# Kernel tuning notes

Measured on AMD Instinct MI355X. Metric: run time of the kernel, lower is better.

The kernel has to match this reference:

```python
import jax, jax.numpy as jnp
import numpy as np

B, N, H = 512, 128, 256      # graphs, nodes per graph, hidden
NH, HD = 8, 32               # heads, head dim
DEG = 8
E = B * N * DEG              # 524288 edges
BN_EPS = 1e-5


def setup_inputs() -> dict:
    key = jax.random.key(0)
    ks = jax.random.split(key, 16)

    def w(k, shape):
        return jax.random.normal(k, shape, dtype=jnp.float32) * 0.02

    # intra-graph random edges: base offset per graph, local src/dst in [0, N)
    base = jnp.repeat(jnp.arange(B, dtype=jnp.int32) * N, N * DEG)
    edge_src = base + jax.random.randint(ks[1], (E,), 0, N, dtype=jnp.int32)
    edge_dst = base + jax.random.randint(ks[2], (E,), 0, N, dtype=jnp.int32)

    return {
        "h": jax.random.normal(ks[0], (B * N, H), dtype=jnp.float32),
        "edge_src": edge_src,
        "edge_dst": edge_dst,
        "gin_w1": w(ks[3], (H, H)), "gin_b1": jnp.zeros((H,), jnp.float32),
        "gin_w2": w(ks[4], (H, H)), "gin_b2": jnp.zeros((H,), jnp.float32),
        "attn_in_w": w(ks[5], (3 * H, H)), "attn_in_b": jnp.zeros((3 * H,), jnp.float32),
        "attn_out_w": w(ks[6], (H, H)), "attn_out_b": jnp.zeros((H,), jnp.float32),
        "bn_local_g": jnp.ones((H,), jnp.float32), "bn_local_b": jnp.zeros((H,), jnp.float32),
        "bn_attn_g": jnp.ones((H,), jnp.float32), "bn_attn_b": jnp.zeros((H,), jnp.float32),
        "bn_out_g": jnp.ones((H,), jnp.float32), "bn_out_b": jnp.zeros((H,), jnp.float32),
        "ffn1_w": w(ks[7], (2 * H, H)), "ffn1_b": jnp.zeros((2 * H,), jnp.float32),
        "ffn2_w": w(ks[8], (H, 2 * H)), "ffn2_b": jnp.zeros((H,), jnp.float32),
    }


def _bn(x, g, b):
    # nn.BatchNorm1d training-mode forward: batch stats over node dim, biased var
    mean = jnp.mean(x, axis=0)
    var = jnp.mean(jnp.square(x - mean), axis=0)
    return g * (x - mean) * jax.lax.rsqrt(var + BN_EPS) + b


def _mha(x, in_w, in_b, out_w, out_b):
    # x: [B, N, H]; uniform graphs -> key_padding_mask is all-valid
    qkv = x @ in_w.T + in_b                           # [B, N, 3H]
    q, k, v = jnp.split(qkv, 3, axis=-1)
    def heads(t):
        return t.reshape(B, N, NH, HD).transpose(0, 2, 1, 3)  # [B, NH, N, HD]
    q, k, v = heads(q), heads(k), heads(v)
    scores = jnp.einsum('bhqd,bhkd->bhqk', q, k) / jnp.sqrt(jnp.float32(HD))
    att = jax.nn.softmax(scores, axis=-1)
    o = jnp.einsum('bhqk,bhkd->bhqd', att, v).transpose(0, 2, 1, 3).reshape(B, N, H)
    return o @ out_w.T + out_b


def reference(h, edge_src, edge_dst,
              gin_w1, gin_b1, gin_w2, gin_b2,
              attn_in_w, attn_in_b, attn_out_w, attn_out_b,
              bn_local_g, bn_local_b, bn_attn_g, bn_attn_b, bn_out_g, bn_out_b,
              ffn1_w, ffn1_b, ffn2_w, ffn2_b):
    # --- local GIN branch: (1+eps)*h + sum_{j in N(i)} h_j, eps=0, then 2-layer MLP
    agg = jax.ops.segment_sum(h[edge_src], edge_dst, num_segments=B * N)
    z = h + agg
    h_local = jax.nn.relu(z @ gin_w1.T + gin_b1) @ gin_w2.T + gin_b2
    h_local = _bn(h + h_local, bn_local_g, bn_local_b)

    # --- global attention branch (to_dense_batch is an exact reshape here)
    h_dense = h.reshape(B, N, H)
    h_attn = _mha(h_dense, attn_in_w, attn_in_b, attn_out_w, attn_out_b).reshape(B * N, H)
    h_attn = _bn(h + h_attn, bn_attn_g, bn_attn_b)

    # --- combine + FFN + out norm
    x = h_local + h_attn
    x = x + jax.nn.relu(x @ ffn1_w.T + ffn1_b) @ ffn2_w.T + ffn2_b
    return _bn(x, bn_out_g, bn_out_b)
```

## Files before the change

kernel.cpp:

```cpp
#include <hip/hip_runtime.h>
#include <hip/hip_bf16.h>

#define B_   512
#define N_   128
#define H_   256
#define NH_  8
#define HD_  32
#define DEG_ 8
#define R_   (B_ * N_)
#define E_   (B_ * N_ * DEG_)
#define EPG_ (N_ * DEG_)

typedef unsigned short u16;
typedef unsigned int u32;

typedef __attribute__((ext_vector_type(8))) short s16x8;
typedef __attribute__((ext_vector_type(4))) float f32x4;

__device__ __forceinline__ float b2f(u16 u) {
  union { u32 i; float f; } v;
  v.i = ((u32)u) << 16;
  return v.f;
}
__device__ __forceinline__ u16 f2b(float f) {
  union { float f; u32 u; } v;
  v.f = f;
  u32 r = (v.u + 0x7fffu + ((v.u >> 16) & 1u)) >> 16;
  return (u16)r;
}
__device__ __forceinline__ void ld4b(const u16* p, float* o) {
  ushort4 v = *(const ushort4*)p;
  o[0] = b2f(v.x); o[1] = b2f(v.y); o[2] = b2f(v.z); o[3] = b2f(v.w);
}

__device__ __forceinline__ int tix(int row, int col) {
  return ((row >> 7) << 15) + (((col >> 6) & 3) << 13) + ((row & 127) << 6) +
         (((((col >> 3) & 7) ^ (row & 7))) << 3) + (col & 7);
}

__device__ __forceinline__ void glds16(const u16* g, u16* l) {
  __builtin_amdgcn_global_load_lds(
      (const __attribute__((address_space(1))) void*)g,
      (__attribute__((address_space(3))) void*)l, 16, 0, 0);
}


#define OFF_GW1 0
#define OFF_GB1 65536
#define OFF_GW2 65792
#define OFF_GB2 131328
#define OFF_AIW 131584
#define OFF_AIB 328192
#define OFF_AOW 328960
#define OFF_AOB 394496
#define OFF_F1W 394752
#define OFF_F1B 525824
#define OFF_F2W 526336
#define OFF_F2B 657408
#define W_TOTAL 657664

__global__ void zero_stats(float* __restrict__ st) {
  st[blockIdx.x * 256 + threadIdx.x] = 0.f;
}

__global__ __launch_bounds__(256) void cvt_h(const float* __restrict__ src,
                                             u16* __restrict__ dst) {
  const int e = (blockIdx.x * 256 + threadIdx.x) * 4;
  const float4 v = *(const float4*)(src + e);
  ushort4 o;
  o.x = f2b(v.x); o.y = f2b(v.y); o.z = f2b(v.z); o.w = f2b(v.w);
  *(ushort4*)(dst + tix(e >> 8, e & 255)) = o;
}

__global__ __launch_bounds__(256) void cvt_w(
    const float* s0, const float* s1, const float* s2, const float* s3,
    const float* s4, const float* s5, const float* s6, const float* s7,
    const float* s8, const float* s9, const float* s10, const float* s11,
    u16* __restrict__ dst) {
  const int sizes[12] = {65536, 256, 65536, 256, 196608, 768,
                         65536, 256, 131072, 512, 131072, 256};
  const float* srcs[12] = {s0, s1, s2, s3, s4, s5, s6, s7, s8, s9, s10, s11};
  int gid = (blockIdx.x * 256 + threadIdx.x) * 4;
  if (gid >= W_TOTAL) return;
  int seg = 0, off = gid;
  while (off >= sizes[seg]) { off -= sizes[seg]; seg++; }
  const float4 v = *(const float4*)(srcs[seg] + off);
  ushort4 o;
  o.x = f2b(v.x); o.y = f2b(v.y); o.z = f2b(v.z); o.w = f2b(v.w);
  *(ushort4*)(dst + gid) = o;
}

#define SROWS_ 32

__global__ __launch_bounds__(256) void agg_kernel(
    const u16* __restrict__ h, const int* __restrict__ esrc,
    const int* __restrict__ edst, u16* __restrict__ z) {
  __shared__ int s_src[EPG_];
  __shared__ int s_cnt[SROWS_];
  __shared__ int s_off[SROWS_ + 1];
  __shared__ int s_pos[SROWS_];
  const int g = blockIdx.x;
  const int r0 = blockIdx.y * SROWS_;
  const int t = threadIdx.x;

  if (t < SROWS_) s_cnt[t] = 0;
  __syncthreads();

  const int ebase = g * EPG_;
  int dl[4], sg[4];
#pragma unroll
  for (int i = 0; i < 4; i++) {
    const int e = ebase + t + i * 256;
    sg[i] = esrc[e];
    dl[i] = edst[e] - g * N_ - r0;
    if ((unsigned)dl[i] < SROWS_) atomicAdd(&s_cnt[dl[i]], 1);
  }
  __syncthreads();
  if (t == 0) {
    int acc = 0;
#pragma unroll
    for (int i = 0; i < SROWS_; i++) { s_off[i] = acc; acc += s_cnt[i]; }
    s_off[SROWS_] = acc;
  }
  __syncthreads();
  if (t < SROWS_) s_pos[t] = s_off[t];
  __syncthreads();
#pragma unroll
  for (int i = 0; i < 4; i++) {
    if ((unsigned)dl[i] < SROWS_) {
      const int slot = atomicAdd(&s_pos[dl[i]], 1);
      s_src[slot] = sg[i];
    }
  }
  __syncthreads();

  const int rg = t >> 5;
  const int c0 = (t & 31) * 8;
  for (int ib = 0; ib < SROWS_; ib += 8) {
    const int i = ib + rg;
    const int row = g * N_ + r0 + i;
    float acc[8];
    {
      const s16x8 v = *(const s16x8*)(h + tix(row, c0));
#pragma unroll
      for (int j = 0; j < 8; j++) acc[j] = b2f((u16)v[j]);
    }
    const int e0 = s_off[i], e1 = s_off[i + 1];
    for (int e = e0; e < e1; e++) {
      const int src = s_src[e];
      const s16x8 v = *(const s16x8*)(h + tix(src, c0));
#pragma unroll
      for (int j = 0; j < 8; j++) acc[j] += b2f((u16)v[j]);
    }
    s16x8 o;
#pragma unroll
    for (int j = 0; j < 8; j++) o[j] = (short)f2b(acc[j]);
    *(s16x8*)(z + tix(row, c0)) = o;
  }
}

template <int NC, int K, int RELU, int RES, int STATS, int ASPLIT, int CMODE>
__global__ __launch_bounds__(256) void gemm_mfma(
    const u16* A, const u16* A2,
    const u16* __restrict__ W, const u16* __restrict__ bias,
    const u16* res, u16* C0, u16* C1, u16* C2,
    float* __restrict__ gsum, float* __restrict__ gsq) {
  __shared__ u16 As[2][64 * 64] __attribute__((aligned(16)));
  __shared__ u16 Bs[2][64 * 64] __attribute__((aligned(16)));

  const int t = threadIdx.x;
  const int wave = t >> 6, lane = t & 63;
  const int wr = wave >> 1, wc = wave & 1;
  const int quad = lane >> 4, ln15 = lane & 15;
  const int row0 = blockIdx.y * 64, col0 = blockIdx.x * 64;

  f32x4 acc[2][2];
#pragma unroll
  for (int i = 0; i < 2; i++)
#pragma unroll
    for (int j = 0; j < 2; j++) acc[i][j] = (f32x4){0.f, 0.f, 0.f, 0.f};

  auto stage = [&](int b, int kt) {
    const u16* Ab;
    int ksl;
    if (ASPLIT) {
      if (kt < 256) { Ab = A; ksl = kt >> 6; } else { Ab = A2; ksl = (kt - 256) >> 6; }
    } else {
      Ab = A; ksl = kt >> 6;
    }
    const u16* abase = Ab + ((size_t)(row0 >> 7) << 15) + (ksl << 13) +
                       ((row0 & 64) << 6);
#pragma unroll
    for (int i = 0; i < 2; i++) {
      const int fid = t + i * 256;
      glds16(abase + fid * 8, &As[b][fid * 8]);
      const int row = fid >> 3;
      const int segp = (fid & 7) ^ (row & 7);
      glds16(W + (size_t)(col0 + row) * K + kt + segp * 8, &Bs[b][fid * 8]);
    }
  };

  stage(0, 0);
  for (int kt = 0; kt < K; kt += 64) {
    const int cur = (kt >> 6) & 1;
    if (kt + 64 < K) {
      stage(cur ^ 1, kt + 64);
      asm volatile("s_waitcnt vmcnt(4)" ::: "memory");
    } else {
      asm volatile("s_waitcnt vmcnt(0)" ::: "memory");
    }
    __builtin_amdgcn_s_barrier();
#pragma unroll
    for (int ks = 0; ks < 64; ks += 32) {
      s16x8 af[2], bf[2];
#pragma unroll
      for (int i = 0; i < 2; i++) {
        const int ra = wr * 32 + i * 16 + ln15;
        af[i] = *(const s16x8*)(
            &As[cur][ra * 64 + ((((ks >> 3) + quad) ^ (ra & 7)) * 8)]);
      }
#pragma unroll
      for (int j = 0; j < 2; j++) {
        const int rb = wc * 32 + j * 16 + ln15;
        bf[j] = *(const s16x8*)(
            &Bs[cur][rb * 64 + ((((ks >> 3) + quad) ^ (rb & 7)) * 8)]);
      }
#pragma unroll
      for (int i = 0; i < 2; i++)
#pragma unroll
        for (int j = 0; j < 2; j++)
          acc[i][j] = __builtin_amdgcn_mfma_f32_16x16x32_bf16(af[i], bf[j], acc[i][j], 0, 0, 0);
    }
    __builtin_amdgcn_s_barrier();
  }

  const int cbase = col0 + wc * 32;
  u16* Cb;
  int coff;
  if (CMODE) {
    const int chunk = col0 >> 8;
    Cb = (chunk == 0) ? C0 : ((chunk == 1) ? C1 : C2);
    coff = (col0 & 255) + wc * 32;
  } else {
    Cb = C0; coff = cbase;
  }

  float bs[2];
#pragma unroll
  for (int j = 0; j < 2; j++) bs[j] = b2f(bias[cbase + j * 16 + ln15]);

  float ssum[2] = {}, ssq[2] = {};
#pragma unroll
  for (int i = 0; i < 2; i++) {
    const int rbase = row0 + wr * 32 + i * 16 + quad * 4;
#pragma unroll
    for (int reg = 0; reg < 4; reg++) {
      const int row = rbase + reg;
#pragma unroll
      for (int j = 0; j < 2; j++) {
        float val = acc[i][j][reg] + bs[j];
        if (RELU) val = fmaxf(val, 0.f);
        if (RES) val += b2f(res[tix(row, cbase + j * 16 + ln15)]);
        Cb[tix(row, coff + j * 16 + ln15)] = f2b(val);
        if (STATS) { ssum[j] += val; ssq[j] += val * val; }
      }
    }
  }

  if (STATS) {
#pragma unroll
    for (int j = 0; j < 2; j++) {
      float s = ssum[j];
      s += __shfl_xor(s, 16);
      s += __shfl_xor(s, 32);
      float q = ssq[j];
      q += __shfl_xor(q, 16);
      q += __shfl_xor(q, 32);
      if (lane < 16) {
        atomicAdd(&gsum[cbase + j * 16 + lane], s);
        atomicAdd(&gsq[cbase + j * 16 + lane], q);
      }
    }
  }
}

template <int CHUNKS, int RES_LDS>
__global__ __launch_bounds__(256, 2) void fused_mlp(
    const u16* A, const u16* __restrict__ W1, const u16* __restrict__ b1,
    const u16* __restrict__ W2, const u16* __restrict__ b2,
    const u16* resg, u16* C,
    float* __restrict__ gsum, float* __restrict__ gsq) {
  __shared__ u16 xs[4 * 64 * 64] __attribute__((aligned(16)));
  __shared__ u16 tc[64 * 128] __attribute__((aligned(16)));
  __shared__ u16 Wst[2][128 * 64] __attribute__((aligned(16)));

  const int t = threadIdx.x;
  const int wave = t >> 6, lane = t & 63;
  const int wr = wave >> 1, wc = wave & 1;
  const int quad = lane >> 4, ln15 = lane & 15;
  const int row0 = blockIdx.x * 64;
  const int K2 = CHUNKS * 128;

  {
    const u16* abase = A + ((size_t)(row0 >> 7) << 15) + ((row0 & 64) << 6);
#pragma unroll
    for (int i = 0; i < 8; i++) {
      const int gid = t + i * 256;
      const int kstep = gid >> 9;
      const int fid = gid & 511;
      glds16(abase + kstep * 8192 + fid * 8, xs + gid * 8);
    }
  }

  f32x4 acc2[2][8];
#pragma unroll
  for (int i = 0; i < 2; i++)
#pragma unroll
    for (int j = 0; j < 8; j++) acc2[i][j] = (f32x4){0.f, 0.f, 0.f, 0.f};

  auto tca = [&](int row, int col) {
    const int s0 = col >> 3;
    return row * 128 + (((s0 & 8) | ((s0 ^ row) & 7)) << 3) + (col & 7);
  };

  for (int c = 0; c < CHUNKS; c++) {
    f32x4 acc1[2][4];
#pragma unroll
    for (int i = 0; i < 2; i++)
#pragma unroll
      for (int j = 0; j < 4; j++) acc1[i][j] = (f32x4){0.f, 0.f, 0.f, 0.f};

    auto stage1 = [&](int b, int kt) {
#pragma unroll
      for (int i = 0; i < 4; i++) {
        const int fid = t + i * 256;
        const int row = fid >> 3;
        const int segp = (fid & 7) ^ (row & 7);
        glds16(W1 + (size_t)(c * 128 + row) * 256 + kt + segp * 8,
               &Wst[b][fid * 8]);
      }
    };

    stage1(0, 0);
    for (int kt = 0; kt < 256; kt += 64) {
      const int cur = (kt >> 6) & 1;
      if (kt + 64 < 256) {
        stage1(cur ^ 1, kt + 64);
        asm volatile("s_waitcnt vmcnt(4)" ::: "memory");
      } else {
        asm volatile("s_waitcnt vmcnt(0)" ::: "memory");
      }
      __builtin_amdgcn_s_barrier();
#pragma unroll
      for (int ks = 0; ks < 64; ks += 32) {
        s16x8 af[2], bf[4];
#pragma unroll
        for (int i = 0; i < 2; i++) {
          const int ra = wr * 32 + i * 16 + ln15;
          af[i] = *(const s16x8*)(
              &xs[(kt >> 6) * 4096 + ra * 64 +
                  ((((ks >> 3) + quad) ^ (ra & 7)) * 8)]);
        }
#pragma unroll
        for (int j = 0; j < 4; j++) {
          const int rb = wc * 64 + j * 16 + ln15;
          bf[j] = *(const s16x8*)(
              &Wst[cur][rb * 64 + ((((ks >> 3) + quad) ^ (rb & 7)) * 8)]);
        }
#pragma unroll
        for (int i = 0; i < 2; i++)
#pragma unroll
          for (int j = 0; j < 4; j++)
            acc1[i][j] = __builtin_amdgcn_mfma_f32_16x16x32_bf16(af[i], bf[j], acc1[i][j], 0, 0, 0);
      }
      __builtin_amdgcn_s_barrier();
    }

    {
      float b1s[4];
#pragma unroll
      for (int j = 0; j < 4; j++)
        b1s[j] = b2f(b1[c * 128 + wc * 64 + j * 16 + ln15]);
#pragma unroll
      for (int i = 0; i < 2; i++)
#pragma unroll
        for (int reg = 0; reg < 4; reg++) {
          const int rowl = wr * 32 + i * 16 + quad * 4 + reg;
#pragma unroll
          for (int j = 0; j < 4; j++) {
            const int coll = wc * 64 + j * 16 + ln15;
            tc[tca(rowl, coll)] = f2b(fmaxf(acc1[i][j][reg] + b1s[j], 0.f));
          }
        }
    }
    __syncthreads();

    for (int ks2 = 0; ks2 < 2; ks2++) {
#pragma unroll
      for (int i = 0; i < 8; i++) {
        const int fid = t + i * 256;
        const int row = fid >> 3;
        const int segp = (fid & 7) ^ (row & 7);
        glds16(W2 + (size_t)row * K2 + c * 128 + ks2 * 64 + segp * 8,
               &Wst[0][fid * 8]);
      }
      asm volatile("s_waitcnt vmcnt(0)" ::: "memory");
      __builtin_amdgcn_s_barrier();
#pragma unroll
      for (int ksl = 0; ksl < 64; ksl += 32) {
        s16x8 af[2], bf[8];
#pragma unroll
        for (int i = 0; i < 2; i++) {
          const int ra = wr * 32 + i * 16 + ln15;
          af[i] = *(const s16x8*)(&tc[tca(ra, ks2 * 64 + ksl + quad * 8)]);
        }
#pragma unroll
        for (int j = 0; j < 8; j++) {
          const int rb = wc * 128 + j * 16 + ln15;
          bf[j] = *(const s16x8*)(
              &Wst[0][rb * 64 + ((((ksl >> 3) + quad) ^ (rb & 7)) * 8)]);
        }
#pragma unroll
        for (int i = 0; i < 2; i++)
#pragma unroll
          for (int j = 0; j < 8; j++)
            acc2[i][j] = __builtin_amdgcn_mfma_f32_16x16x32_bf16(af[i], bf[j], acc2[i][j], 0, 0, 0);
      }
      __builtin_amdgcn_s_barrier();
    }
  }

  float bs2[8];
#pragma unroll
  for (int j = 0; j < 8; j++)
    bs2[j] = b2f(b2[wc * 128 + j * 16 + ln15]);

  float ssum[8] = {}, ssq[8] = {};
#pragma unroll
  for (int i = 0; i < 2; i++) {
#pragma unroll
    for (int reg = 0; reg < 4; reg++) {
      const int rowl = wr * 32 + i * 16 + quad * 4 + reg;
      const int row = row0 + rowl;
#pragma unroll
      for (int j = 0; j < 8; j++) {
        const int col = wc * 128 + j * 16 + ln15;
        float val = acc2[i][j][reg] + bs2[j];
        if (RES_LDS) {
          val += b2f(xs[(col >> 6) * 4096 + rowl * 64 +
                        ((((col >> 3) & 7) ^ (rowl & 7)) << 3) + (col & 7)]);
        } else {
          val += b2f(resg[tix(row, col)]);
        }
        C[tix(row, col)] = f2b(val);
        ssum[j] += val; ssq[j] += val * val;
      }
    }
  }

#pragma unroll
  for (int j = 0; j < 8; j++) {
    float s = ssum[j];
    s += __shfl_xor(s, 16);
    s += __shfl_xor(s, 32);
    float q = ssq[j];
    q += __shfl_xor(q, 16);
    q += __shfl_xor(q, 32);
    if (lane < 16) {
      atomicAdd(&gsum[wc * 128 + j * 16 + lane], s);
      atomicAdd(&gsq[wc * 128 + j * 16 + lane], q);
    }
  }
}

__global__ __launch_bounds__(256) void attn_mfma(
    const u16* q, const u16* __restrict__ k,
    const u16* __restrict__ v, u16* o) {
  __shared__ u16 lds[21760] __attribute__((aligned(16)));
  u16* Vt = lds;
  u16* Qs = lds + 4352;
  u16* Ks = lds + 4352 + 5120;
  u16* P  = lds + 4352;

  const int g = blockIdx.x >> 3;
  const int hd = blockIdx.x & 7;
  const int t = threadIdx.x;
  const int wave = t >> 6, lane = t & 63;
  const int quad = lane >> 4, ln15 = lane & 15;
  const int strip = wave * 32;
  const float scale = 0.1767766952966369f;

#pragma unroll
  for (int i = 0; i < 4; i++) {
    const int fid = t + i * 256;
    const int row = fid >> 3;
    const int seg = fid & 7;
    const int gidx = tix(g * N_ + row, hd * HD_ + seg * 4);
    const ushort4 qv = *(const ushort4*)(q + gidx);
    const ushort4 kv = *(const ushort4*)(k + gidx);
    const ushort4 vv = *(const ushort4*)(v + gidx);
    ushort4 qs;
    qs.x = f2b(b2f(qv.x) * scale); qs.y = f2b(b2f(qv.y) * scale);
    qs.z = f2b(b2f(qv.z) * scale); qs.w = f2b(b2f(qv.w) * scale);
    *(ushort4*)(Qs + row * 40 + seg * 4) = qs;
    *(ushort4*)(Ks + row * 40 + seg * 4) = kv;
    Vt[(seg * 4 + 0) * 136 + row] = vv.x;
    Vt[(seg * 4 + 1) * 136 + row] = vv.y;
    Vt[(seg * 4 + 2) * 136 + row] = vv.z;
    Vt[(seg * 4 + 3) * 136 + row] = vv.w;
  }
  __syncthreads();

  s16x8 af[2], bf[8];
#pragma unroll
  for (int mi = 0; mi < 2; mi++)
    af[mi] = *(const s16x8*)(Qs + (strip + mi * 16 + ln15) * 40 + quad * 8);
#pragma unroll
  for (int nj = 0; nj < 8; nj++)
    bf[nj] = *(const s16x8*)(Ks + (nj * 16 + ln15) * 40 + quad * 8);

  f32x4 acc[2][8];
#pragma unroll
  for (int mi = 0; mi < 2; mi++)
#pragma unroll
    for (int nj = 0; nj < 8; nj++)
      acc[mi][nj] = __builtin_amdgcn_mfma_f32_16x16x32_bf16(
          af[mi], bf[nj], (f32x4){0.f, 0.f, 0.f, 0.f}, 0, 0, 0);

  __syncthreads();

#pragma unroll
  for (int mi = 0; mi < 2; mi++) {
#pragma unroll
    for (int reg = 0; reg < 4; reg++) {
      float mx = acc[mi][0][reg];
#pragma unroll
      for (int j = 1; j < 8; j++) mx = fmaxf(mx, acc[mi][j][reg]);
      mx = fmaxf(mx, __shfl_xor(mx, 1));
      mx = fmaxf(mx, __shfl_xor(mx, 2));
      mx = fmaxf(mx, __shfl_xor(mx, 4));
      mx = fmaxf(mx, __shfl_xor(mx, 8));
      float e[8], s = 0.f;
#pragma unroll
      for (int j = 0; j < 8; j++) { e[j] = __expf(acc[mi][j][reg] - mx); s += e[j]; }
      s += __shfl_xor(s, 1);
      s += __shfl_xor(s, 2);
      s += __shfl_xor(s, 4);
      s += __shfl_xor(s, 8);
      const float inv = 1.f / s;
      const int prow = strip + mi * 16 + quad * 4 + reg;
#pragma unroll
      for (int j = 0; j < 8; j++)
        P[prow * 136 + j * 16 + ln15] = f2b(e[j] * inv);
    }
  }
  __syncthreads();

  f32x4 acc2[2][2];
#pragma unroll
  for (int mi = 0; mi < 2; mi++)
#pragma unroll
    for (int nj = 0; nj < 2; nj++) acc2[mi][nj] = (f32x4){0.f, 0.f, 0.f, 0.f};
#pragma unroll
  for (int kt = 0; kt < 4; kt++) {
    s16x8 paf[2], vbf[2];
#pragma unroll
    for (int mi = 0; mi < 2; mi++)
      paf[mi] = *(const s16x8*)(P + (strip + mi * 16 + ln15) * 136 + kt * 32 + quad * 8);
#pragma unroll
    for (int nj = 0; nj < 2; nj++)
      vbf[nj] = *(const s16x8*)(Vt + (nj * 16 + ln15) * 136 + kt * 32 + quad * 8);
#pragma unroll
    for (int mi = 0; mi < 2; mi++)
#pragma unroll
      for (int nj = 0; nj < 2; nj++)
        acc2[mi][nj] = __builtin_amdgcn_mfma_f32_16x16x32_bf16(
            paf[mi], vbf[nj], acc2[mi][nj], 0, 0, 0);
  }

#pragma unroll
  for (int mi = 0; mi < 2; mi++)
#pragma unroll
    for (int nj = 0; nj < 2; nj++)
#pragma unroll
      for (int reg = 0; reg < 4; reg++) {
        const int row = strip + mi * 16 + quad * 4 + reg;
        o[tix(g * N_ + row, hd * HD_ + nj * 16 + ln15)] =
            f2b(acc2[mi][nj][reg]);
      }
}

__global__ void bn_finalize(const float* __restrict__ sum,
                            const float* __restrict__ sq,
                            const float* __restrict__ g,
                            const float* __restrict__ bb,
                            float* __restrict__ a, float* __restrict__ b) {
  const int c = threadIdx.x;
  const float mean = sum[c] * (1.f / R_);
  const float var = fmaxf(sq[c] * (1.f / R_) - mean * mean, 0.f);
  const float ai = g[c] * rsqrtf(var + 1e-5f);
  a[c] = ai;
  b[c] = bb[c] - mean * ai;
}

__global__ __launch_bounds__(256) void combine_kernel(
    const u16* __restrict__ rl, const u16* __restrict__ ra,
    const float* __restrict__ st, u16* __restrict__ x) {
  const int e = (blockIdx.x * 256 + threadIdx.x) * 4;
  const int col = e & 255;
  const int idx = tix(e >> 8, col);
  float rl4[4], ra4[4];
  ld4b(rl + idx, rl4);
  ld4b(ra + idx, ra4);
  const float* al = st + 1536;
  const float* bl = st + 1792;
  const float* aa = st + 2048;
  const float* ba = st + 2304;
  ushort4 o;
  u16* ov = (u16*)&o;
#pragma unroll
  for (int j = 0; j < 4; j++)
    ov[j] = f2b(al[col + j] * rl4[j] + bl[col + j] + aa[col + j] * ra4[j] + ba[col + j]);
  *(ushort4*)(x + idx) = o;
}

__global__ __launch_bounds__(256) void final_kernel(
    const u16* __restrict__ y, const float* __restrict__ st,
    float* __restrict__ out) {
  const int e = (blockIdx.x * 256 + threadIdx.x) * 4;
  const int col = e & 255;
  float y4[4];
  ld4b(y + tix(e >> 8, col), y4);
  const float* ao = st + 2560;
  const float* bo = st + 2816;
  float4 o;
  o.x = ao[col + 0] * y4[0] + bo[col + 0];
  o.y = ao[col + 1] * y4[1] + bo[col + 1];
  o.z = ao[col + 2] * y4[2] + bo[col + 2];
  o.w = ao[col + 3] * y4[3] + bo[col + 3];
  *(float4*)(out + e) = o;
}

extern "C" void kernel_launch(void* const* d_in, const int* in_sizes, int n_in,
                              void* d_out, int out_size, void* d_ws, size_t ws_size,
                              hipStream_t stream) {
  const float* h = (const float*)d_in[0];
  const int* esrc = (const int*)d_in[1];
  const int* edst = (const int*)d_in[2];
  const float* bn_local_g = (const float*)d_in[11];
  const float* bn_local_b = (const float*)d_in[12];
  const float* bn_attn_g = (const float*)d_in[13];
  const float* bn_attn_b = (const float*)d_in[14];
  const float* bn_out_g = (const float*)d_in[15];
  const float* bn_out_b = (const float*)d_in[16];

  const size_t RH = (size_t)R_ * H_;
  float* stats = (float*)d_ws;
  u16* WB = (u16*)((char*)d_ws + 65536);
  u16* Hb = (u16*)((char*)d_ws + 65536 + 2097152);
  u16* S1 = Hb + RH;
  u16* S2 = S1 + RH;
  u16* OD = (u16*)d_out;
  float* outf = (float*)d_out;

  zero_stats<<<12, 256, 0, stream>>>(stats);
  cvt_h<<<(int)(RH / 4 / 256), 256, 0, stream>>>(h, Hb);
  cvt_w<<<(W_TOTAL / 4 + 255) / 256, 256, 0, stream>>>(
      (const float*)d_in[3], (const float*)d_in[4], (const float*)d_in[5],
      (const float*)d_in[6], (const float*)d_in[7], (const float*)d_in[8],
      (const float*)d_in[9], (const float*)d_in[10], (const float*)d_in[17],
      (const float*)d_in[18], (const float*)d_in[19], (const float*)d_in[20], WB);

  gemm_mfma<768, 256, 0, 0, 0, 0, 1><<<dim3(12, 1024), 256, 0, stream>>>(
      Hb, nullptr, WB + OFF_AIW, WB + OFF_AIB, nullptr, S1, S2, OD,
      nullptr, nullptr);
  attn_mfma<<<B_ * NH_, 256, 0, stream>>>(S1, S2, OD, S1);
  gemm_mfma<256, 256, 0, 1, 1, 0, 0><<<dim3(4, 1024), 256, 0, stream>>>(
      S1, nullptr, WB + OFF_AOW, WB + OFF_AOB, Hb, S2, nullptr, nullptr,
      stats + 512, stats + 768);
  agg_kernel<<<dim3(B_, 4), 256, 0, stream>>>(Hb, esrc, edst, OD);
  fused_mlp<2, 0><<<1024, 256, 0, stream>>>(
      OD, WB + OFF_GW1, WB + OFF_GB1, WB + OFF_GW2, WB + OFF_GB2, Hb, OD,
      stats + 0, stats + 256);

  bn_finalize<<<1, 256, 0, stream>>>(stats + 0, stats + 256, bn_local_g,
                                     bn_local_b, stats + 1536, stats + 1792);
  bn_finalize<<<1, 256, 0, stream>>>(stats + 512, stats + 768, bn_attn_g,
                                     bn_attn_b, stats + 2048, stats + 2304);

  combine_kernel<<<(int)(RH / 4 / 256), 256, 0, stream>>>(OD, S2, stats, S1);
  fused_mlp<4, 1><<<1024, 256, 0, stream>>>(
      S1, WB + OFF_F1W, WB + OFF_F1B, WB + OFF_F2W, WB + OFF_F2B, nullptr, S1,
      stats + 1024, stats + 1280);

  bn_finalize<<<1, 256, 0, stream>>>(stats + 1024, stats + 1280, bn_out_g,
                                     bn_out_b, stats + 2560, stats + 2816);
  final_kernel<<<(int)(RH / 4 / 256), 256, 0, stream>>>(S1, stats, outf);
}
```

Before: 549.5 us.

## Load MLP weight fragments directly from global memory instead of LDS staging

The fused MLP kernel no longer stages W1/W2 tiles into shared memory with double buffering. Each wave now reads its B-operand fragments straight from global memory, relying on L2/L1 caching. This drops the 32KB Wst buffer and most barriers, which frees shared memory so launch bounds can be raised to 3 blocks per CU. The trade-off is more global/cache traffic per wave, uncoalesced 16-byte row-strided reads, and load latency that is no longer hidden by the explicit pipeline.

```diff
diff --git a/kernel.cpp b/kernel.cpp
--- a/kernel.cpp
+++ b/kernel.cpp
@@ -285,14 +285,13 @@
 }
 
 template <int CHUNKS, int RES_LDS>
-__global__ __launch_bounds__(256, 2) void fused_mlp(
+__global__ __launch_bounds__(256, 3) void fused_mlp(
     const u16* A, const u16* __restrict__ W1, const u16* __restrict__ b1,
     const u16* __restrict__ W2, const u16* __restrict__ b2,
     const u16* resg, u16* C,
     float* __restrict__ gsum, float* __restrict__ gsq) {
   __shared__ u16 xs[4 * 64 * 64] __attribute__((aligned(16)));
   __shared__ u16 tc[64 * 128] __attribute__((aligned(16)));
-  __shared__ u16 Wst[2][128 * 64] __attribute__((aligned(16)));
 
   const int t = threadIdx.x;
   const int wave = t >> 6, lane = t & 63;
@@ -311,6 +310,8 @@
       glds16(abase + kstep * 8192 + fid * 8, xs + gid * 8);
     }
   }
+  asm volatile("s_waitcnt vmcnt(0)" ::: "memory");
+  __builtin_amdgcn_s_barrier();
 
   f32x4 acc2[2][8];
 #pragma unroll
@@ -330,50 +331,26 @@
 #pragma unroll
       for (int j = 0; j < 4; j++) acc1[i][j] = (f32x4){0.f, 0.f, 0.f, 0.f};
 
-    auto stage1 = [&](int b, int kt) {
-#pragma unroll
-      for (int i = 0; i < 4; i++) {
-        const int fid = t + i * 256;
-        const int row = fid >> 3;
-        const int segp = (fid & 7) ^ (row & 7);
-        glds16(W1 + (size_t)(c * 128 + row) * 256 + kt + segp * 8,
-               &Wst[b][fid * 8]);
-      }
-    };
-
-    stage1(0, 0);
-    for (int kt = 0; kt < 256; kt += 64) {
-      const int cur = (kt >> 6) & 1;
-      if (kt + 64 < 256) {
-        stage1(cur ^ 1, kt + 64);
-        asm volatile("s_waitcnt vmcnt(4)" ::: "memory");
-      } else {
-        asm volatile("s_waitcnt vmcnt(0)" ::: "memory");
-      }
-      __builtin_amdgcn_s_barrier();
-#pragma unroll
-      for (int ks = 0; ks < 64; ks += 32) {
-        s16x8 af[2], bf[4];
-#pragma unroll
-        for (int i = 0; i < 2; i++) {
-          const int ra = wr * 32 + i * 16 + ln15;
-          af[i] = *(const s16x8*)(
-              &xs[(kt >> 6) * 4096 + ra * 64 +
-                  ((((ks >> 3) + quad) ^ (ra & 7)) * 8)]);
-        }
-#pragma unroll
-        for (int j = 0; j < 4; j++) {
-          const int rb = wc * 64 + j * 16 + ln15;
-          bf[j] = *(const s16x8*)(
-              &Wst[cur][rb * 64 + ((((ks >> 3) + quad) ^ (rb & 7)) * 8)]);
-        }
-#pragma unroll
-        for (int i = 0; i < 2; i++)
-#pragma unroll
-          for (int j = 0; j < 4; j++)
-            acc1[i][j] = __builtin_amdgcn_mfma_f32_16x16x32_bf16(af[i], bf[j], acc1[i][j], 0, 0, 0);
-      }
-      __builtin_amdgcn_s_barrier();
+#pragma unroll
+    for (int ks = 0; ks < 256; ks += 32) {
+      s16x8 af[2], bf[4];
+#pragma unroll
+      for (int i = 0; i < 2; i++) {
+        const int ra = wr * 32 + i * 16 + ln15;
+        af[i] = *(const s16x8*)(
+            &xs[(ks >> 6) * 4096 + ra * 64 +
+                (((((ks & 63) >> 3) + quad) ^ (ra & 7)) * 8)]);
+      }
+#pragma unroll
+      for (int j = 0; j < 4; j++) {
+        const int grow = c * 128 + wc * 64 + j * 16 + ln15;
+        bf[j] = *(const s16x8*)(W1 + (size_t)grow * 256 + ks + quad * 8);
+      }
+#pragma unroll
+      for (int i = 0; i < 2; i++)
+#pragma unroll
+        for (int j = 0; j < 4; j++)
+          acc1[i][j] = __builtin_amdgcn_mfma_f32_16x16x32_bf16(af[i], bf[j], acc1[i][j], 0, 0, 0);
     }
 
     {
@@ -395,39 +372,26 @@
     }
     __syncthreads();
 
-    for (int ks2 = 0; ks2 < 2; ks2++) {
-#pragma unroll
-      for (int i = 0; i < 8; i++) {
-        const int fid = t + i * 256;
-        const int row = fid >> 3;
-        const int segp = (fid & 7) ^ (row & 7);
-        glds16(W2 + (size_t)row * K2 + c * 128 + ks2 * 64 + segp * 8,
-               &Wst[0][fid * 8]);
-      }
-      asm volatile("s_waitcnt vmcnt(0)" ::: "memory");
-      __builtin_amdgcn_s_barrier();
-#pragma unroll
-      for (int ksl = 0; ksl < 64; ksl += 32) {
-        s16x8 af[2], bf[8];
-#pragma unroll
-        for (int i = 0; i < 2; i++) {
-          const int ra = wr * 32 + i * 16 + ln15;
-          af[i] = *(const s16x8*)(&tc[tca(ra, ks2 * 64 + ksl + quad * 8)]);
-        }
-#pragma unroll
-        for (int j = 0; j < 8; j++) {
-          const int rb = wc * 128 + j * 16 + ln15;
-          bf[j] = *(const s16x8*)(
-              &Wst[0][rb * 64 + ((((ksl >> 3) + quad) ^ (rb & 7)) * 8)]);
-        }
-#pragma unroll
-        for (int i = 0; i < 2; i++)
-#pragma unroll
-          for (int j = 0; j < 8; j++)
-            acc2[i][j] = __builtin_amdgcn_mfma_f32_16x16x32_bf16(af[i], bf[j], acc2[i][j], 0, 0, 0);
-      }
-      __builtin_amdgcn_s_barrier();
-    }
+#pragma unroll
+    for (int ks2 = 0; ks2 < 128; ks2 += 32) {
+      s16x8 af[2], bf[8];
+#pragma unroll
+      for (int i = 0; i < 2; i++) {
+        const int ra = wr * 32 + i * 16 + ln15;
+        af[i] = *(const s16x8*)(&tc[tca(ra, ks2 + quad * 8)]);
+      }
+#pragma unroll
+      for (int j = 0; j < 8; j++) {
+        const int grow = wc * 128 + j * 16 + ln15;
+        bf[j] = *(const s16x8*)(W2 + (size_t)grow * K2 + c * 128 + ks2 + quad * 8);
+      }
+#pragma unroll
+      for (int i = 0; i < 2; i++)
+#pragma unroll
+        for (int j = 0; j < 8; j++)
+          acc2[i][j] = __builtin_amdgcn_mfma_f32_16x16x32_bf16(af[i], bf[j], acc2[i][j], 0, 0, 0);
+    }
+    __syncthreads();
   }
 
   float bs2[8];
```

Measured after the change: 741.1 us. 34.9% more time.
